# Performance work log

Hardware: AMD Instinct MI355X
Metric: run time of the kernel (lower is better)

Reference implementation:

```python
import jax, jax.numpy as jnp
import numpy as np

NUM_HEADS = 16
HEAD_DIM = 64
WINDOW = 512  # attention_window; band half-width = WINDOW // 2
MAX_TIME = 10000.0  # rotary default max timescale


def apply_rotary(x):
    """Rotary encoding as in pos_encs_lib.apply_rotary_encoding.

    x: [b, t, h, d]. Pairs (x[2i], x[2i+1]) are rotated by angle pos * inv_freq,
    with inv_freq repeated per pair (interleaved layout).
    """
    d = x.shape[-1]
    freq_seq = jnp.arange(d // 2, dtype=jnp.float32) / (d // 2)
    inv_freq = jnp.repeat(MAX_TIME ** -freq_seq, 2)  # [d]
    pos = jnp.arange(x.shape[1], dtype=jnp.float32)
    t = pos[None, :, None, None] * inv_freq[None, None, None, :]  # [1,t,1,d]
    xp = x.reshape(*x.shape[:-1], d // 2, 2)
    x_rot = jnp.stack([-xp[..., 1], xp[..., 0]], axis=-1).reshape(x.shape)
    return x * jnp.cos(t).astype(x.dtype) + x_rot * jnp.sin(t).astype(x.dtype)


def setup_inputs() -> dict:
    key = jax.random.key(0)
    ks = jax.random.split(key, 6)
    B, T, E = 4, 2048, 1024
    H = NUM_HEADS * HEAD_DIM
    return {
        "inputs_q": jax.random.normal(ks[0], (B, T, E), jnp.float32),
        "inputs_kv": jax.random.normal(ks[1], (B, T, E), jnp.float32),
        "Wq": jax.random.normal(ks[2], (E, H), jnp.float32) * 0.02,
        "Wk": jax.random.normal(ks[3], (E, H), jnp.float32) * 0.02,
        "Wv": jax.random.normal(ks[4], (E, H), jnp.float32) * 0.02,
        "Wo": jax.random.normal(ks[5], (H, E), jnp.float32) * 0.02,
    }


def reference(inputs_q, inputs_kv, Wq, Wk, Wv, Wo):
    b, T, E = inputs_q.shape
    q = (inputs_q @ Wq).reshape(b, T, NUM_HEADS, HEAD_DIM)
    k = (inputs_kv @ Wk).reshape(b, T, NUM_HEADS, HEAD_DIM)
    v = (inputs_kv @ Wv).reshape(b, T, NUM_HEADS, HEAD_DIM)
    q = apply_rotary(q)
    k = apply_rotary(k)
    # [b, h, t, T] attention logits, scaled by 1/sqrt(head_dim)
    att = jnp.einsum('bthd,bThd->bhtT', q, k) * (1.0 / np.sqrt(HEAD_DIM))
    # sliding-window band mask: |i - j| <= WINDOW // 2 (matches k-diagonal sum)
    idx = jnp.arange(T)
    band = jnp.abs(idx[:, None] - idx[None, :]) <= (WINDOW // 2)
    att = jnp.where(band, att, jnp.finfo(jnp.float32).min)
    p = jax.nn.softmax(att, axis=-1)
    out = jnp.einsum('bhtT,bThd->bthd', p, v).reshape(b, T, NUM_HEADS * HEAD_DIM)
    return out @ Wo
```

## Files before the change

kernel.cpp:

```cpp
#include <hip/hip_runtime.h>


typedef __attribute__((ext_vector_type(8))) short s8v;
typedef __attribute__((ext_vector_type(4))) float f4v;

#define MFMA_BF16 __builtin_amdgcn_mfma_f32_16x16x32_bf16

#define ASYNC_CP16(g, l)                                             \
  __builtin_amdgcn_global_load_lds(                                  \
      (const __attribute__((address_space(1))) void*)(g),            \
      (__attribute__((address_space(3))) void*)(l), 16, 0, 0)

#define SWZ(row, g) ((row) * 64 + ((((g) ^ ((row) & 7))) * 8))

__device__ __forceinline__ unsigned short f2bf(float f) {
  union { float f; unsigned int u; } v; v.f = f;
  unsigned int r = (v.u + 0x7fffu + ((v.u >> 16) & 1u)) >> 16;
  return (unsigned short)r;
}

__global__ __launch_bounds__(256) void cvt2_kernel(
    const float* __restrict__ s0, const float* __restrict__ s1,
    unsigned short* __restrict__ d0, unsigned short* __restrict__ d1) {
  int g = blockIdx.x;
  const float* src = (g < 8192) ? s0 : s1;
  unsigned short* dst = (g < 8192) ? d0 : d1;
  int i = ((g & 8191) * 256 + threadIdx.x) * 4;
  float4 v = *(const float4*)(src + i);
  ushort4 o;
  o.x = f2bf(v.x); o.y = f2bf(v.y); o.z = f2bf(v.z); o.w = f2bf(v.w);
  *(ushort4*)(dst + i) = o;
}

__global__ __launch_bounds__(256) void wtrans_kernel(
    const float* __restrict__ W0, const float* __restrict__ W1,
    const float* __restrict__ W2, const float* __restrict__ W3,
    unsigned short* __restrict__ D0, unsigned short* __restrict__ D1,
    unsigned short* __restrict__ D2, unsigned short* __restrict__ D3) {
  const float* W = blockIdx.z == 0 ? W0 : blockIdx.z == 1 ? W1 : blockIdx.z == 2 ? W2 : W3;
  unsigned short* D = blockIdx.z == 0 ? D0 : blockIdx.z == 1 ? D1 : blockIdx.z == 2 ? D2 : D3;
  __shared__ float tile[32][33];
  int n0 = blockIdx.x * 32, k0 = blockIdx.y * 32;
  int tx = threadIdx.x & 31, ty = threadIdx.x >> 5;
#pragma unroll
  for (int r = 0; r < 32; r += 8)
    tile[ty + r][tx] = W[(size_t)(k0 + ty + r) * 1024 + n0 + tx];
  __syncthreads();
#pragma unroll
  for (int r = 0; r < 32; r += 8)
    D[(size_t)(n0 + ty + r) * 1024 + k0 + tx] = f2bf(tile[tx][ty + r]);
}

__global__ __launch_bounds__(256) void proj_gemm(
    const unsigned short* __restrict__ XqBf, const unsigned short* __restrict__ XkvBf,
    const unsigned short* __restrict__ Wtq, const unsigned short* __restrict__ Wtk,
    const unsigned short* __restrict__ Wtv,
    unsigned short* __restrict__ Qb, unsigned short* __restrict__ Kb,
    unsigned short* __restrict__ Vt) {
  const int K = 1024;
  int z = blockIdx.z;
  const unsigned short* A  = (z == 0) ? XqBf : XkvBf;
  const unsigned short* Bt = (z == 0) ? Wtq : (z == 1) ? Wtk : Wtv;

  __shared__ __align__(16) unsigned short sA[128 * 64];
  __shared__ __align__(16) unsigned short sB[128 * 64];

  int tid = threadIdx.x;
  int lane = tid & 63, wave = tid >> 6;
  int quad = lane >> 4, l16 = lane & 15;
  int wm = wave & 1, wn = wave >> 1;
  int m_blk = blockIdx.x * 128, n_blk = blockIdx.y * 128;

  f4v acc[4][4] = {};
  int srow = tid >> 3, sg = (tid & 7) ^ (srow & 7);
  const unsigned short* gA = A + (size_t)(m_blk + srow) * K + sg * 8;
  const unsigned short* gB = Bt + (size_t)(n_blk + srow) * K + sg * 8;

  for (int k0 = 0; k0 < K; k0 += 64) {
#pragma unroll
    for (int i = 0; i < 4; ++i) {
      ASYNC_CP16(gA + (size_t)i * 32 * K + k0, &sA[i * 2048 + tid * 8]);
      ASYNC_CP16(gB + (size_t)i * 32 * K + k0, &sB[i * 2048 + tid * 8]);
    }
    __syncthreads();
#pragma unroll
    for (int ks = 0; ks < 64; ks += 32) {
      s8v af[4], bf[4];
#pragma unroll
      for (int mt = 0; mt < 4; ++mt)
        af[mt] = *(const s8v*)&sA[SWZ(wm * 64 + mt * 16 + l16, quad + (ks >> 3))];
#pragma unroll
      for (int nt = 0; nt < 4; ++nt)
        bf[nt] = *(const s8v*)&sB[SWZ(wn * 64 + nt * 16 + l16, quad + (ks >> 3))];
#pragma unroll
      for (int mt = 0; mt < 4; ++mt)
#pragma unroll
        for (int nt = 0; nt < 4; ++nt)
          acc[mt][nt] = MFMA_BF16(af[mt], bf[nt], acc[mt][nt], 0, 0, 0);
    }
    __syncthreads();
  }

  if (z < 2) {
    unsigned short* Cb = (z == 0) ? Qb : Kb;
#pragma unroll
    for (int mt = 0; mt < 4; ++mt)
#pragma unroll
      for (int nt = 0; nt < 4; ++nt)
#pragma unroll
        for (int r = 0; r < 4; ++r) {
          int row = m_blk + wm * 64 + mt * 16 + quad * 4 + r;
          int col = n_blk + wn * 64 + nt * 16 + l16;
          float v = acc[mt][nt][r];
          float other = __shfl_xor(v, 1);
          int dh = col & 63;
          int tpos = row & 2047;
          float fi = (float)(dh >> 1) * (1.0f / 32.0f);
          float invf = __expf(-9.210340371976184f * fi);
          float ang = (float)tpos * invf;
          float s, c;
          __sincosf(ang, &s, &c);
          v = (dh & 1) ? (v * c + other * s) : (v * c - other * s);
          Cb[(size_t)row * 1024 + col] = f2bf(v);
        }
  } else {
#pragma unroll
    for (int mt = 0; mt < 4; ++mt)
#pragma unroll
      for (int nt = 0; nt < 4; ++nt) {
        int row0 = m_blk + wm * 64 + mt * 16 + quad * 4;
        int col = n_blk + wn * 64 + nt * 16 + l16;
        int bb = row0 >> 11, t = row0 & 2047;
        int hh = col >> 6, dh = col & 63;
        ushort4 pk;
        pk.x = f2bf(acc[mt][nt][0]);
        pk.y = f2bf(acc[mt][nt][1]);
        pk.z = f2bf(acc[mt][nt][2]);
        pk.w = f2bf(acc[mt][nt][3]);
        *(ushort4*)&Vt[(((size_t)bb * 16 + hh) * 64 + dh) * 2048 + t] = pk;
      }
  }
}

__global__ __launch_bounds__(256) void attn_kernel(
    const unsigned short* __restrict__ Qb, const unsigned short* __restrict__ Kb,
    const unsigned short* __restrict__ Vt, unsigned short* __restrict__ Ab) {
  const int T = 2048;
  int t0 = blockIdx.x * 128;
  int h = blockIdx.y, b = blockIdx.z;
  int tid = threadIdx.x, lane = tid & 63, wave = tid >> 6;
  int quad = lane >> 4, l16 = lane & 15;

  __shared__ __align__(16) unsigned short sQP[128][72];
  __shared__ __align__(16) unsigned short sK[64][72];
  __shared__ __align__(16) unsigned short sV[64][72];

  size_t base = ((size_t)b * T) * 1024 + (size_t)h * 64;
  size_t vbase = ((size_t)b * 16 + h) * 64 * 2048;

  {
    int qr = tid >> 1, qc = (tid & 1) * 32;
    const unsigned short* g = Qb + base + (size_t)(t0 + qr) * 1024 + qc;
#pragma unroll
    for (int j = 0; j < 4; ++j)
      *(uint4*)&sQP[qr][qc + j * 8] = *(const uint4*)(g + j * 8);
  }
  s8v aq[2][2];
#pragma unroll
  for (int f = 0; f < 2; ++f) {
    aq[f][0] = *(const s8v*)&sQP[wave * 32 + f * 16 + l16][quad * 8];
    aq[f][1] = *(const s8v*)&sQP[wave * 32 + f * 16 + l16][32 + quad * 8];
  }

  f4v oacc[2][4] = {};
  float mrow[2][4], lrow[2][4];
#pragma unroll
  for (int f = 0; f < 2; ++f)
#pragma unroll
    for (int r = 0; r < 4; ++r) { mrow[f][r] = -1e30f; lrow[f][r] = 0.0f; }

  int kv_lo = max(0, t0 - 256);
  int kv_hi = min(T, t0 + 128 + 256);
  int ntiles = (kv_hi - kv_lo) >> 6;

  int srow = tid >> 2, sseg = (tid & 3) * 16;
  const unsigned short* gK = Kb + base + (size_t)(kv_lo + srow) * 1024 + sseg;
  const unsigned short* gV = Vt + vbase + (size_t)srow * 2048 + kv_lo + sseg;
  uint4 rk0 = *(const uint4*)gK, rk1 = *(const uint4*)(gK + 8);
  uint4 rv0 = *(const uint4*)gV, rv1 = *(const uint4*)(gV + 8);

  int qlo = t0 + wave * 32;

  for (int it = 0; it < ntiles; ++it) {
    int kv0 = kv_lo + (it << 6);
    __syncthreads();
    *(uint4*)&sK[srow][sseg] = rk0;
    *(uint4*)&sK[srow][sseg + 8] = rk1;
    *(uint4*)&sV[srow][sseg] = rv0;
    *(uint4*)&sV[srow][sseg + 8] = rv1;
    __syncthreads();
    if (it + 1 < ntiles) {
      const unsigned short* nK = gK + (size_t)(it + 1) * 64 * 1024;
      const unsigned short* nV = gV + (it + 1) * 64;
      rk0 = *(const uint4*)nK; rk1 = *(const uint4*)(nK + 8);
      rv0 = *(const uint4*)nV; rv1 = *(const uint4*)(nV + 8);
    }
    if (kv0 > qlo + 31 + 256 || kv0 + 63 < qlo - 256) continue;

#pragma unroll
    for (int f = 0; f < 2; ++f) {
      f4v sacc[4];
#pragma unroll
      for (int nt = 0; nt < 4; ++nt) {
        s8v b0 = *(const s8v*)&sK[nt * 16 + l16][quad * 8];
        s8v b1 = *(const s8v*)&sK[nt * 16 + l16][32 + quad * 8];
        f4v zz = {};
        zz = MFMA_BF16(aq[f][0], b0, zz, 0, 0, 0);
        sacc[nt] = MFMA_BF16(aq[f][1], b1, zz, 0, 0, 0);
      }

      int qg = qlo + f * 16 + quad * 4;
      float p[4][4];
      float mx[4];
#pragma unroll
      for (int r = 0; r < 4; ++r) mx[r] = -1e30f;
#pragma unroll
      for (int nt = 0; nt < 4; ++nt) {
        int kg = kv0 + nt * 16 + l16;
#pragma unroll
        for (int r = 0; r < 4; ++r) {
          int d = qg + r - kg;
          float s = sacc[nt][r] * 0.125f;
          s = (d <= 256 && d >= -256) ? s : -1e30f;
          p[nt][r] = s;
          mx[r] = fmaxf(mx[r], s);
        }
      }
#pragma unroll
      for (int off = 1; off < 16; off <<= 1)
#pragma unroll
        for (int r = 0; r < 4; ++r) mx[r] = fmaxf(mx[r], __shfl_xor(mx[r], off));

      float alpha[4], rsum[4];
#pragma unroll
      for (int r = 0; r < 4; ++r) {
        float mn = fmaxf(mrow[f][r], mx[r]);
        alpha[r] = __expf(mrow[f][r] - mn);
        mrow[f][r] = mn;
        rsum[r] = 0.0f;
      }
#pragma unroll
      for (int nt = 0; nt < 4; ++nt)
#pragma unroll
        for (int r = 0; r < 4; ++r) {
          float e = __expf(p[nt][r] - mrow[f][r]);
          p[nt][r] = e;
          rsum[r] += e;
        }
#pragma unroll
      for (int off = 1; off < 16; off <<= 1)
#pragma unroll
        for (int r = 0; r < 4; ++r) rsum[r] += __shfl_xor(rsum[r], off);
#pragma unroll
      for (int r = 0; r < 4; ++r) {
        lrow[f][r] = lrow[f][r] * alpha[r] + rsum[r];
#pragma unroll
        for (int dt = 0; dt < 4; ++dt) oacc[f][dt][r] *= alpha[r];
      }

#pragma unroll
      for (int nt = 0; nt < 4; ++nt)
#pragma unroll
        for (int r = 0; r < 4; ++r)
          sQP[wave * 32 + f * 16 + quad * 4 + r][nt * 16 + l16] = f2bf(p[nt][r]);
      s8v pa0 = *(const s8v*)&sQP[wave * 32 + f * 16 + l16][quad * 8];
      s8v pa1 = *(const s8v*)&sQP[wave * 32 + f * 16 + l16][32 + quad * 8];

#pragma unroll
      for (int dt = 0; dt < 4; ++dt) {
        s8v bv0 = *(const s8v*)&sV[dt * 16 + l16][quad * 8];
        s8v bv1 = *(const s8v*)&sV[dt * 16 + l16][32 + quad * 8];
        oacc[f][dt] = MFMA_BF16(pa0, bv0, oacc[f][dt], 0, 0, 0);
        oacc[f][dt] = MFMA_BF16(pa1, bv1, oacc[f][dt], 0, 0, 0);
      }
    }
  }

#pragma unroll
  for (int f = 0; f < 2; ++f) {
    float inv_l[4];
#pragma unroll
    for (int r = 0; r < 4; ++r) inv_l[r] = 1.0f / lrow[f][r];
#pragma unroll
    for (int dt = 0; dt < 4; ++dt)
#pragma unroll
      for (int r = 0; r < 4; ++r) {
        int row = t0 + wave * 32 + f * 16 + quad * 4 + r;
        int col = dt * 16 + l16;
        Ab[base + (size_t)row * 1024 + col] = f2bf(oacc[f][dt][r] * inv_l[r]);
      }
  }
}

__global__ __launch_bounds__(256) void out_gemm(
    const unsigned short* __restrict__ A, const unsigned short* __restrict__ Bt,
    float* __restrict__ C) {
  const int K = 1024;
  __shared__ __align__(16) unsigned short sA[128 * 64];
  __shared__ __align__(16) unsigned short sB[128 * 64];

  int tid = threadIdx.x;
  int lane = tid & 63, wave = tid >> 6;
  int quad = lane >> 4, l16 = lane & 15;
  int wm = wave & 1, wn = wave >> 1;
  int m_blk = blockIdx.x * 128, n_blk = blockIdx.y * 128;

  f4v acc[4][4] = {};
  int srow = tid >> 3, sg = (tid & 7) ^ (srow & 7);
  const unsigned short* gA = A + (size_t)(m_blk + srow) * K + sg * 8;
  const unsigned short* gB = Bt + (size_t)(n_blk + srow) * K + sg * 8;

  for (int k0 = 0; k0 < K; k0 += 64) {
#pragma unroll
    for (int i = 0; i < 4; ++i) {
      ASYNC_CP16(gA + (size_t)i * 32 * K + k0, &sA[i * 2048 + tid * 8]);
      ASYNC_CP16(gB + (size_t)i * 32 * K + k0, &sB[i * 2048 + tid * 8]);
    }
    __syncthreads();
#pragma unroll
    for (int ks = 0; ks < 64; ks += 32) {
      s8v af[4], bf[4];
#pragma unroll
      for (int mt = 0; mt < 4; ++mt)
        af[mt] = *(const s8v*)&sA[SWZ(wm * 64 + mt * 16 + l16, quad + (ks >> 3))];
#pragma unroll
      for (int nt = 0; nt < 4; ++nt)
        bf[nt] = *(const s8v*)&sB[SWZ(wn * 64 + nt * 16 + l16, quad + (ks >> 3))];
#pragma unroll
      for (int mt = 0; mt < 4; ++mt)
#pragma unroll
        for (int nt = 0; nt < 4; ++nt)
          acc[mt][nt] = MFMA_BF16(af[mt], bf[nt], acc[mt][nt], 0, 0, 0);
    }
    __syncthreads();
  }

#pragma unroll
  for (int mt = 0; mt < 4; ++mt)
#pragma unroll
    for (int nt = 0; nt < 4; ++nt)
#pragma unroll
      for (int r = 0; r < 4; ++r) {
        int row = m_blk + wm * 64 + mt * 16 + quad * 4 + r;
        int col = n_blk + wn * 64 + nt * 16 + l16;
        C[(size_t)row * 1024 + col] = acc[mt][nt][r];
      }
}

extern "C" void kernel_launch(void* const* d_in, const int* in_sizes, int n_in,
                              void* d_out, int out_size, void* d_ws, size_t ws_size,
                              hipStream_t stream) {
  const float* Xq  = (const float*)d_in[0];
  const float* Xkv = (const float*)d_in[1];
  const float* Wq  = (const float*)d_in[2];
  const float* Wk  = (const float*)d_in[3];
  const float* Wv  = (const float*)d_in[4];
  const float* Wo  = (const float*)d_in[5];
  float* out = (float*)d_out;

  char* ws = (char*)d_ws;
  const size_t MB = 1ull << 20;
  unsigned short* XqBf  = (unsigned short*)(ws + 0 * MB);
  unsigned short* XkvBf = (unsigned short*)(ws + 16 * MB);
  unsigned short* Wtq   = (unsigned short*)(ws + 32 * MB);
  unsigned short* Wtk   = (unsigned short*)(ws + 34 * MB);
  unsigned short* Wtv   = (unsigned short*)(ws + 36 * MB);
  unsigned short* Wto   = (unsigned short*)(ws + 38 * MB);
  unsigned short* Qb    = (unsigned short*)(ws + 40 * MB);
  unsigned short* Kb    = (unsigned short*)(ws + 56 * MB);
  unsigned short* Vt    = (unsigned short*)(ws + 72 * MB);
  unsigned short* Ab    = XqBf;

  cvt2_kernel<<<16384, 256, 0, stream>>>(Xq, Xkv, XqBf, XkvBf);
  wtrans_kernel<<<dim3(32, 32, 4), 256, 0, stream>>>(Wq, Wk, Wv, Wo, Wtq, Wtk, Wtv, Wto);
  proj_gemm<<<dim3(64, 8, 3), 256, 0, stream>>>(XqBf, XkvBf, Wtq, Wtk, Wtv, Qb, Kb, Vt);
  attn_kernel<<<dim3(16, 16, 4), 256, 0, stream>>>(Qb, Kb, Vt, Ab);
  out_gemm<<<dim3(64, 8), 256, 0, stream>>>(Ab, Wto, out);
}
```

Before: 293.8 us.

## Transpose attention MFMAs so each lane owns a query row, fold scale into Q

The attention kernel swaps MFMA operand order so scores come out transposed (keys along registers, queries along lanes). Each lane then holds one query row's softmax state, which cuts the per-row max/sum shuffle reductions to two shuffles and turns mrow/lrow into scalars. Q is loaded directly from global into registers instead of going through shared memory, and the 1/sqrt(d) scale is folded into the Q projection epilogue. Band masking is skipped for tiles lying fully inside the window, P is written packed to a smaller per-wave shared buffer, output stores are vectorised, and launch bounds request 4 blocks per CU. This trades some extra register pressure and a bf16 rounding of the pre-scaled Q for fewer shuffles, less LDS traffic and cheaper softmax bookkeeping.

```diff
diff --git a/kernel.cpp b/kernel.cpp
--- a/kernel.cpp
+++ b/kernel.cpp
@@ -1,4 +1,5 @@
 #include <hip/hip_runtime.h>
+#include <hip/hip_bf16.h>
 
 
 typedef __attribute__((ext_vector_type(8))) short s8v;
@@ -17,6 +18,12 @@
   union { float f; unsigned int u; } v; v.f = f;
   unsigned int r = (v.u + 0x7fffu + ((v.u >> 16) & 1u)) >> 16;
   return (unsigned short)r;
+}
+
+__device__ __forceinline__ unsigned int pack_bf16(float a, float b) {
+  union { __hip_bfloat162 h; unsigned int u; } cv;
+  cv.h = __float22bfloat162_rn(make_float2(a, b));
+  return cv.u;
 }
 
 __global__ __launch_bounds__(256) void cvt2_kernel(
@@ -103,6 +110,7 @@
 
   if (z < 2) {
     unsigned short* Cb = (z == 0) ? Qb : Kb;
+    float post = (z == 0) ? 0.125f : 1.0f;
 #pragma unroll
     for (int mt = 0; mt < 4; ++mt)
 #pragma unroll
@@ -121,7 +129,7 @@
           float s, c;
           __sincosf(ang, &s, &c);
           v = (dh & 1) ? (v * c + other * s) : (v * c - other * s);
-          Cb[(size_t)row * 1024 + col] = f2bf(v);
+          Cb[(size_t)row * 1024 + col] = f2bf(v * post);
         }
   } else {
 #pragma unroll
@@ -142,7 +150,7 @@
   }
 }
 
-__global__ __launch_bounds__(256) void attn_kernel(
+__global__ __launch_bounds__(256, 4) void attn_kernel(
     const unsigned short* __restrict__ Qb, const unsigned short* __restrict__ Kb,
     const unsigned short* __restrict__ Vt, unsigned short* __restrict__ Ab) {
   const int T = 2048;
@@ -151,33 +159,24 @@
   int tid = threadIdx.x, lane = tid & 63, wave = tid >> 6;
   int quad = lane >> 4, l16 = lane & 15;
 
-  __shared__ __align__(16) unsigned short sQP[128][72];
   __shared__ __align__(16) unsigned short sK[64][72];
   __shared__ __align__(16) unsigned short sV[64][72];
+  __shared__ __align__(16) unsigned short sP[4][16][72];
 
   size_t base = ((size_t)b * T) * 1024 + (size_t)h * 64;
   size_t vbase = ((size_t)b * 16 + h) * 64 * 2048;
-
-  {
-    int qr = tid >> 1, qc = (tid & 1) * 32;
-    const unsigned short* g = Qb + base + (size_t)(t0 + qr) * 1024 + qc;
-#pragma unroll
-    for (int j = 0; j < 4; ++j)
-      *(uint4*)&sQP[qr][qc + j * 8] = *(const uint4*)(g + j * 8);
-  }
-  s8v aq[2][2];
+  int qlo = t0 + wave * 32;
+
+  s8v bq[2][2];
 #pragma unroll
   for (int f = 0; f < 2; ++f) {
-    aq[f][0] = *(const s8v*)&sQP[wave * 32 + f * 16 + l16][quad * 8];
-    aq[f][1] = *(const s8v*)&sQP[wave * 32 + f * 16 + l16][32 + quad * 8];
+    const unsigned short* g = Qb + base + (size_t)(qlo + f * 16 + l16) * 1024;
+    bq[f][0] = *(const s8v*)(g + quad * 8);
+    bq[f][1] = *(const s8v*)(g + 32 + quad * 8);
   }
 
   f4v oacc[2][4] = {};
-  float mrow[2][4], lrow[2][4];
-#pragma unroll
-  for (int f = 0; f < 2; ++f)
-#pragma unroll
-    for (int r = 0; r < 4; ++r) { mrow[f][r] = -1e30f; lrow[f][r] = 0.0f; }
+  float mrow[2] = {-1e30f, -1e30f}, lrow[2] = {0.0f, 0.0f};
 
   int kv_lo = max(0, t0 - 256);
   int kv_hi = min(T, t0 + 128 + 256);
@@ -189,8 +188,6 @@
   uint4 rk0 = *(const uint4*)gK, rk1 = *(const uint4*)(gK + 8);
   uint4 rv0 = *(const uint4*)gV, rv1 = *(const uint4*)(gV + 8);
 
-  int qlo = t0 + wave * 32;
-
   for (int it = 0; it < ntiles; ++it) {
     int kv0 = kv_lo + (it << 6);
     __syncthreads();
@@ -209,96 +206,83 @@
 
 #pragma unroll
     for (int f = 0; f < 2; ++f) {
+      int qf = qlo + f * 16;
+      int qg = qf + l16;
       f4v sacc[4];
 #pragma unroll
       for (int nt = 0; nt < 4; ++nt) {
-        s8v b0 = *(const s8v*)&sK[nt * 16 + l16][quad * 8];
-        s8v b1 = *(const s8v*)&sK[nt * 16 + l16][32 + quad * 8];
+        s8v ak0 = *(const s8v*)&sK[nt * 16 + l16][quad * 8];
+        s8v ak1 = *(const s8v*)&sK[nt * 16 + l16][32 + quad * 8];
         f4v zz = {};
-        zz = MFMA_BF16(aq[f][0], b0, zz, 0, 0, 0);
-        sacc[nt] = MFMA_BF16(aq[f][1], b1, zz, 0, 0, 0);
-      }
-
-      int qg = qlo + f * 16 + quad * 4;
-      float p[4][4];
-      float mx[4];
-#pragma unroll
-      for (int r = 0; r < 4; ++r) mx[r] = -1e30f;
+        zz = MFMA_BF16(ak0, bq[f][0], zz, 0, 0, 0);
+        sacc[nt] = MFMA_BF16(ak1, bq[f][1], sacc[nt] = zz, 0, 0, 0);
+      }
+      bool full = (kv0 >= qf - 241) && (kv0 <= qf + 193);
+      if (!full) {
+#pragma unroll
+        for (int nt = 0; nt < 4; ++nt) {
+          int kg = kv0 + nt * 16 + quad * 4;
+#pragma unroll
+          for (int r = 0; r < 4; ++r) {
+            int d = qg - (kg + r);
+            if (d > 256 || d < -256) sacc[nt][r] = -1e30f;
+          }
+        }
+      }
+      float mymax = sacc[0][0];
+#pragma unroll
+      for (int nt = 0; nt < 4; ++nt)
+#pragma unroll
+        for (int r = 0; r < 4; ++r) mymax = fmaxf(mymax, sacc[nt][r]);
+      mymax = fmaxf(mymax, __shfl_xor(mymax, 16));
+      mymax = fmaxf(mymax, __shfl_xor(mymax, 32));
+
+      float mn = fmaxf(mrow[f], mymax);
+      float alpha = __expf(mrow[f] - mn);
+      mrow[f] = mn;
+
+      float mysum = 0.0f;
 #pragma unroll
       for (int nt = 0; nt < 4; ++nt) {
-        int kg = kv0 + nt * 16 + l16;
-#pragma unroll
-        for (int r = 0; r < 4; ++r) {
-          int d = qg + r - kg;
-          float s = sacc[nt][r] * 0.125f;
-          s = (d <= 256 && d >= -256) ? s : -1e30f;
-          p[nt][r] = s;
-          mx[r] = fmaxf(mx[r], s);
-        }
-      }
-#pragma unroll
-      for (int off = 1; off < 16; off <<= 1)
-#pragma unroll
-        for (int r = 0; r < 4; ++r) mx[r] = fmaxf(mx[r], __shfl_xor(mx[r], off));
-
-      float alpha[4], rsum[4];
-#pragma unroll
-      for (int r = 0; r < 4; ++r) {
-        float mn = fmaxf(mrow[f][r], mx[r]);
-        alpha[r] = __expf(mrow[f][r] - mn);
-        mrow[f][r] = mn;
-        rsum[r] = 0.0f;
-      }
-#pragma unroll
-      for (int nt = 0; nt < 4; ++nt)
-#pragma unroll
-        for (int r = 0; r < 4; ++r) {
-          float e = __expf(p[nt][r] - mrow[f][r]);
-          p[nt][r] = e;
-          rsum[r] += e;
-        }
-#pragma unroll
-      for (int off = 1; off < 16; off <<= 1)
-#pragma unroll
-        for (int r = 0; r < 4; ++r) rsum[r] += __shfl_xor(rsum[r], off);
-#pragma unroll
-      for (int r = 0; r < 4; ++r) {
-        lrow[f][r] = lrow[f][r] * alpha[r] + rsum[r];
-#pragma unroll
-        for (int dt = 0; dt < 4; ++dt) oacc[f][dt][r] *= alpha[r];
-      }
-
-#pragma unroll
-      for (int nt = 0; nt < 4; ++nt)
-#pragma unroll
-        for (int r = 0; r < 4; ++r)
-          sQP[wave * 32 + f * 16 + quad * 4 + r][nt * 16 + l16] = f2bf(p[nt][r]);
-      s8v pa0 = *(const s8v*)&sQP[wave * 32 + f * 16 + l16][quad * 8];
-      s8v pa1 = *(const s8v*)&sQP[wave * 32 + f * 16 + l16][32 + quad * 8];
+        float e0 = __expf(sacc[nt][0] - mn);
+        float e1 = __expf(sacc[nt][1] - mn);
+        float e2 = __expf(sacc[nt][2] - mn);
+        float e3 = __expf(sacc[nt][3] - mn);
+        mysum += (e0 + e1) + (e2 + e3);
+        *(uint2*)&sP[wave][l16][nt * 16 + quad * 4] =
+            make_uint2(pack_bf16(e0, e1), pack_bf16(e2, e3));
+      }
+      mysum += __shfl_xor(mysum, 16);
+      mysum += __shfl_xor(mysum, 32);
+      lrow[f] = lrow[f] * alpha + mysum;
+
+      s8v pb0 = *(const s8v*)&sP[wave][l16][quad * 8];
+      s8v pb1 = *(const s8v*)&sP[wave][l16][32 + quad * 8];
 
 #pragma unroll
       for (int dt = 0; dt < 4; ++dt) {
-        s8v bv0 = *(const s8v*)&sV[dt * 16 + l16][quad * 8];
-        s8v bv1 = *(const s8v*)&sV[dt * 16 + l16][32 + quad * 8];
-        oacc[f][dt] = MFMA_BF16(pa0, bv0, oacc[f][dt], 0, 0, 0);
-        oacc[f][dt] = MFMA_BF16(pa1, bv1, oacc[f][dt], 0, 0, 0);
+        s8v av0 = *(const s8v*)&sV[dt * 16 + l16][quad * 8];
+        s8v av1 = *(const s8v*)&sV[dt * 16 + l16][32 + quad * 8];
+        f4v o = oacc[f][dt];
+#pragma unroll
+        for (int r = 0; r < 4; ++r) o[r] *= alpha;
+        o = MFMA_BF16(av0, pb0, o, 0, 0, 0);
+        oacc[f][dt] = MFMA_BF16(av1, pb1, o, 0, 0, 0);
       }
     }
   }
 
 #pragma unroll
   for (int f = 0; f < 2; ++f) {
-    float inv_l[4];
-#pragma unroll
-    for (int r = 0; r < 4; ++r) inv_l[r] = 1.0f / lrow[f][r];
-#pragma unroll
-    for (int dt = 0; dt < 4; ++dt)
-#pragma unroll
-      for (int r = 0; r < 4; ++r) {
-        int row = t0 + wave * 32 + f * 16 + quad * 4 + r;
-        int col = dt * 16 + l16;
-        Ab[base + (size_t)row * 1024 + col] = f2bf(oacc[f][dt][r] * inv_l[r]);
-      }
+    float inv = 1.0f / lrow[f];
+    size_t rowoff = base + (size_t)(qlo + f * 16 + l16) * 1024;
+#pragma unroll
+    for (int dt = 0; dt < 4; ++dt) {
+      float o0 = oacc[f][dt][0] * inv, o1 = oacc[f][dt][1] * inv;
+      float o2 = oacc[f][dt][2] * inv, o3 = oacc[f][dt][3] * inv;
+      *(uint2*)&Ab[rowoff + dt * 16 + quad * 4] =
+          make_uint2(pack_bf16(o0, o1), pack_bf16(o2, o3));
+    }
   }
 }
 
```

After: 259.0 us. 11.8% less time.
